# Kernel optimization log

Measured on AMD Instinct MI355X. Metric: run time of the kernel, lower is better.

Reference implementation:

```python
import jax, jax.numpy as jnp
import numpy as np

N = 100000   # nodes (batched graph)
E = 1600000  # edges
G = 2048     # molecules in the batch
D_IN = 128
D_H = 128
MLP_H = 512


def setup_inputs() -> dict:
    key = jax.random.key(0)
    ks = jax.random.split(key, 20)

    def w(k, i, o):
        return (jax.random.normal(k, (i, o), jnp.float32) / np.sqrt(i)).astype(jnp.float32)

    feats = jax.random.normal(ks[0], (N, D_IN), jnp.float32)
    src = jax.random.randint(ks[1], (E,), 0, N)
    dst = jax.random.randint(ks[2], (E,), 0, N)
    graph_ids = jnp.sort(jax.random.randint(ks[3], (N,), 0, G))

    return {
        "feats": feats, "src": src, "dst": dst, "graph_ids": graph_ids,
        # 3 GraphConv layers
        "W0": w(ks[4], D_IN, D_H), "b0": jnp.zeros((D_H,), jnp.float32),
        "W1": w(ks[5], D_H, D_H),  "b1": jnp.zeros((D_H,), jnp.float32),
        "W2": w(ks[6], D_H, D_H),  "b2": jnp.zeros((D_H,), jnp.float32),
        # MLP head: D_H -> 512 -> 256 -> 1
        "Wm0": w(ks[7], D_H, MLP_H),       "bm0": jnp.zeros((MLP_H,), jnp.float32),
        "Wm1": w(ks[8], MLP_H, MLP_H // 2), "bm1": jnp.zeros((MLP_H // 2,), jnp.float32),
        "Wm2": w(ks[9], MLP_H // 2, 1),     "bm2": jnp.zeros((1,), jnp.float32),
    }


def reference(feats, src, dst, graph_ids, W0, b0, W1, b1, W2, b2,
              Wm0, bm0, Wm1, bm1, Wm2, bm2):
    ones_e = jnp.ones((E,), jnp.float32)
    # DGL GraphConv norm='both': D_out^{-1/2} on src, D_in^{-1/2} on dst; deg clamped to 1
    deg_out = jnp.maximum(jax.ops.segment_sum(ones_e, src, num_segments=N), 1.0)
    deg_in = jnp.maximum(jax.ops.segment_sum(ones_e, dst, num_segments=N), 1.0)
    inv_src = jax.lax.rsqrt(deg_out)[:, None]
    inv_dst = jax.lax.rsqrt(deg_in)[:, None]

    def gcn_layer(h, W, b):
        h = h * inv_src                                   # [N, D]
        m = jax.ops.segment_sum(h[src], dst, num_segments=N)  # gather-scatter over edges
        m = m * inv_dst
        return jax.nn.relu(jnp.dot(m, W) + b)

    h = gcn_layer(feats, W0, b0)
    h = gcn_layer(h, W1, b1)
    h = gcn_layer(h, W2, b2)

    # AvgPooling per graph
    counts = jnp.maximum(jax.ops.segment_sum(jnp.ones((N,), jnp.float32), graph_ids, num_segments=G), 1.0)
    emb = jax.ops.segment_sum(h, graph_ids, num_segments=G) / counts[:, None]  # [G, D_H]

    # MLP head (dropout = identity in eval)
    x = jax.nn.relu(jnp.dot(emb, Wm0) + bm0)
    x = jax.nn.relu(jnp.dot(x, Wm1) + bm1)
    return jnp.dot(x, Wm2) + bm2  # [G, 1]
```

## Files before the change

kernel.cpp:

```cpp
#include <hip/hip_runtime.h>


static inline int ceil_div(int a, int b){ return (a + b - 1) / b; }

#define B1 256
#define NBMAX 1024
#define CHUNK_MAX 7168
#define BUCKET_MAX 4096
#define WPREP_BLOCKS 192

typedef __bf16 bf16x8 __attribute__((ext_vector_type(8)));
typedef float  f32x4  __attribute__((ext_vector_type(4)));

static __device__ inline __bf16 bits_to_bf16(unsigned short u){
  union { unsigned short u; __bf16 b; } x; x.u = u; return x.b;
}
static __device__ inline unsigned short bf16_bits(__bf16 b){
  union { __bf16 b; unsigned short u; } x; x.b = b; return x.u;
}
static __device__ inline unsigned pack_split(float s){
  __bf16 h = (__bf16)s;
  __bf16 l = (__bf16)(s - (float)h);
  return ((unsigned)bf16_bits(h) << 16) | (unsigned)bf16_bits(l);
}

__global__ __launch_bounds__(256) void scatter_count_kernel(
    const int* __restrict__ src, const int* __restrict__ dst,
    unsigned* __restrict__ cntA, unsigned* __restrict__ cntB,
    unsigned* __restrict__ stagedA, unsigned char* __restrict__ stagedB,
    const float* __restrict__ W0, const float* __restrict__ W1,
    const float* __restrict__ W2, __bf16* __restrict__ Wsp,
    int E, int NB){
  if (blockIdx.x >= B1){
    int gidx = (blockIdx.x - B1)*256 + threadIdx.x;
    if (gidx < 3*128*128){
      int layer = gidx >> 14, idx = gidx & 16383;
      const float* W = layer == 0 ? W0 : (layer == 1 ? W1 : W2);
      int k = idx >> 7, n = idx & 127;
      float w = W[idx];
      __bf16 h = (__bf16)w;
      __bf16 l = (__bf16)(w - (float)h);
      Wsp[(size_t)layer*2*16384 + n*128 + k] = h;
      Wsp[(size_t)layer*2*16384 + 16384 + n*128 + k] = l;
    }
    return;
  }

  __shared__ unsigned la[NBMAX], lb[NBMAX];
  __shared__ unsigned tsum[256];
  __shared__ unsigned stA[CHUNK_MAX];
  __shared__ unsigned char stB[CHUNK_MAX];

  const int t = threadIdx.x;
  const int blk = blockIdx.x;
  const int chunk = (E + B1 - 1) / B1;
  const int e0 = blk * chunk, e1 = min(e0 + chunk, E);
  const int len = e1 - e0;
  const int strideB = (chunk + 3) & ~3;

  #pragma unroll
  for (int i = t; i < NBMAX; i += 256){ la[i] = 0u; lb[i] = 0u; }
  __syncthreads();
  for (int e = e0 + t; e < e1; e += 256){
    atomicAdd(&la[dst[e] >> 7], 1u);
    atomicAdd(&lb[src[e] >> 7], 1u);
  }
  __syncthreads();

  for (int job = 0; job < 2; job++){
    unsigned* lx = job ? lb : la;
    unsigned* cx = job ? cntB : cntA;
    int b4 = t*4;
    unsigned v0 = lx[b4], v1 = lx[b4+1], v2 = lx[b4+2], v3 = lx[b4+3];
    unsigned s = v0+v1+v2+v3;
    tsum[t] = s;
    __syncthreads();
    for (int off = 1; off < 256; off <<= 1){
      unsigned u = (t >= off) ? tsum[t-off] : 0u;
      __syncthreads();
      tsum[t] += u;
      __syncthreads();
    }
    unsigned run = tsum[t] - s;
    unsigned o0 = run, o1 = run+v0, o2 = run+v0+v1, o3 = run+v0+v1+v2;
    lx[b4] = o0; lx[b4+1] = o1; lx[b4+2] = o2; lx[b4+3] = o3;
    if (b4   < NB) cx[(size_t)blk*NB + b4  ] = o0;
    if (b4+1 < NB) cx[(size_t)blk*NB + b4+1] = o1;
    if (b4+2 < NB) cx[(size_t)blk*NB + b4+2] = o2;
    if (b4+3 < NB) cx[(size_t)blk*NB + b4+3] = o3;
    __syncthreads();
  }

  for (int e = e0 + t; e < e1; e += 256){
    int s = src[e], d = dst[e];
    unsigned pA = atomicAdd(&la[d >> 7], 1u);
    stA[pA] = ((unsigned)(d & 127) << 17) | (unsigned)s;
    unsigned pB = atomicAdd(&lb[s >> 7], 1u);
    stB[pB] = (unsigned char)(s & 127);
  }
  __syncthreads();

  for (int i = t; i < len; i += 256)
    stagedA[(size_t)blk*chunk + i] = stA[i];
  int w4 = (len + 3) >> 2;
  unsigned* gB = (unsigned*)(stagedB + (size_t)blk*strideB);
  for (int i = t; i < w4; i += 256)
    gB[i] = *(unsigned*)&stB[4*i];
}

__global__ void totals_kernel(const unsigned* __restrict__ cntA,
                              const unsigned* __restrict__ cntB,
                              unsigned* __restrict__ totals, int NB, int E){
  int b = blockIdx.x * 256 + threadIdx.x;
  if (b >= NB) return;
  const unsigned* cx = blockIdx.y ? cntB : cntA;
  const int chunk = (E + B1 - 1) / B1;
  unsigned run = 0;
  for (int blk = 0; blk < B1; blk++){
    int lenb = E - blk*chunk; if (lenb > chunk) lenb = chunk; if (lenb < 0) lenb = 0;
    unsigned cur = cx[(size_t)blk*NB + b];
    unsigned nxt = (b < NB-1) ? cx[(size_t)blk*NB + b + 1] : (unsigned)lenb;
    run += nxt - cur;
  }
  totals[(size_t)blockIdx.y*NB + b] = run;
}

__global__ void scan_base_kernel(const unsigned* __restrict__ totals,
                                 unsigned* __restrict__ baseA, unsigned* __restrict__ baseB,
                                 int NB, int E){
  __shared__ unsigned s[NBMAX];
  int t = threadIdx.x;
  for (int job = 0; job < 2; job++){
    unsigned* base = job ? baseB : baseA;
    unsigned x = (t < NB) ? totals[(size_t)job*NB + t] : 0u;
    s[t] = x;
    __syncthreads();
    for (int off = 1; off < NBMAX; off <<= 1){
      unsigned v = (t >= off) ? s[t - off] : 0u;
      __syncthreads();
      s[t] += v;
      __syncthreads();
    }
    if (t < NB) base[t] = s[t] - x;
    if (t == 0) base[NB] = (unsigned)E;
    __syncthreads();
  }
}

__global__ __launch_bounds__(256) void csr_finalize_kernel(
    const unsigned* __restrict__ stagedA, const unsigned char* __restrict__ stagedB,
    const unsigned* __restrict__ cntA, const unsigned* __restrict__ cntB,
    const unsigned* __restrict__ baseA,
    int* __restrict__ row_ptr, float* __restrict__ inv_dst, float* __restrict__ inv_src,
    int* __restrict__ col, int N, int E, int NB){
  __shared__ unsigned offs[256];
  __shared__ unsigned segbase[257];
  __shared__ unsigned tsum[256];
  __shared__ unsigned edge[BUCKET_MAX];
  __shared__ unsigned sorted[BUCKET_MAX];
  __shared__ unsigned cnt[128];
  __shared__ unsigned scn[128];

  const int b = blockIdx.x, t = threadIdx.x;
  const int node0 = b << 7;
  const int nn = min(128, N - node0);
  const int chunk = (E + B1 - 1) / B1;
  const int strideB = (chunk + 3) & ~3;
  int lenb_t = E - t*chunk; if (lenb_t > chunk) lenb_t = chunk; if (lenb_t < 0) lenb_t = 0;

  {
    unsigned o0 = cntA[(size_t)t*NB + b];
    unsigned o1 = (b < NB-1) ? cntA[(size_t)t*NB + b + 1] : (unsigned)lenb_t;
    unsigned len = o1 - o0;
    offs[t] = o0;
    tsum[t] = len;
    __syncthreads();
    for (int off = 1; off < 256; off <<= 1){
      unsigned u = (t >= off) ? tsum[t-off] : 0u;
      __syncthreads();
      tsum[t] += u;
      __syncthreads();
    }
    segbase[t] = tsum[t] - len;
    if (t == 255) segbase[256] = tsum[255];
    __syncthreads();
    int bucketlen = (int)segbase[256];

    for (int idx = t; idx < bucketlen; idx += 256){
      int lo = 0, hi = 255;
      while (lo < hi){ int m = (lo + hi + 1) >> 1; if (segbase[m] <= (unsigned)idx) lo = m; else hi = m - 1; }
      edge[idx] = stagedA[(size_t)lo*chunk + offs[lo] + ((unsigned)idx - segbase[lo])];
    }
    if (t < 128) cnt[t] = 0u;
    __syncthreads();
    for (int idx = t; idx < bucketlen; idx += 256)
      atomicAdd(&cnt[(edge[idx] >> 17) & 127u], 1u);
    __syncthreads();
    unsigned mycnt = (t < 128) ? cnt[t] : 0u;
    if (t < 128) scn[t] = mycnt;
    __syncthreads();
    for (int off = 1; off < 128; off <<= 1){
      unsigned v = (t < 128 && t >= off) ? scn[t - off] : 0u;
      __syncthreads();
      if (t < 128) scn[t] += v;
      __syncthreads();
    }
    int e0 = (int)baseA[b];
    if (t < nn){
      unsigned excl = scn[t] - mycnt;
      row_ptr[node0 + t] = e0 + (int)excl;
      unsigned c = mycnt < 1u ? 1u : mycnt;
      inv_dst[node0 + t] = rsqrtf((float)c);
      cnt[t] = excl;
    }
    if (b == NB - 1 && t == 0) row_ptr[N] = E;
    __syncthreads();
    for (int idx = t; idx < bucketlen; idx += 256){
      unsigned v = edge[idx];
      unsigned p = atomicAdd(&cnt[(v >> 17) & 127u], 1u);
      sorted[p] = v & 0x1FFFFu;
    }
    __syncthreads();
    for (int idx = t; idx < bucketlen; idx += 256)
      col[e0 + idx] = (int)sorted[idx];
  }

  __syncthreads();
  {
    unsigned o0 = cntB[(size_t)t*NB + b];
    unsigned o1 = (b < NB-1) ? cntB[(size_t)t*NB + b + 1] : (unsigned)lenb_t;
    unsigned len = o1 - o0;
    offs[t] = o0;
    tsum[t] = len;
    __syncthreads();
    for (int off = 1; off < 256; off <<= 1){
      unsigned u = (t >= off) ? tsum[t-off] : 0u;
      __syncthreads();
      tsum[t] += u;
      __syncthreads();
    }
    segbase[t] = tsum[t] - len;
    if (t == 255) segbase[256] = tsum[255];
    if (t < 128) cnt[t] = 0u;
    __syncthreads();
    int bucketlen = (int)segbase[256];
    unsigned char* edgeB = (unsigned char*)edge;
    for (int idx = t; idx < bucketlen; idx += 256){
      int lo = 0, hi = 255;
      while (lo < hi){ int m = (lo + hi + 1) >> 1; if (segbase[m] <= (unsigned)idx) lo = m; else hi = m - 1; }
      edgeB[idx] = stagedB[(size_t)lo*strideB + offs[lo] + ((unsigned)idx - segbase[lo])];
    }
    __syncthreads();
    for (int idx = t; idx < bucketlen; idx += 256)
      atomicAdd(&cnt[edgeB[idx]], 1u);
    __syncthreads();
    if (t < nn){
      unsigned c = cnt[t] < 1u ? 1u : cnt[t];
      inv_src[node0 + t] = rsqrtf((float)c);
    }
  }
}

template<bool SC>
__global__ __launch_bounds__(512) void fused_agg_gemm_kernel(
    const int* __restrict__ row_ptr, const int* __restrict__ col,
    const float* __restrict__ hs_in, const float* __restrict__ scale,
    const float* __restrict__ inv_dst,
    const __bf16* __restrict__ Whi, const __bf16* __restrict__ Wlo,
    const float* __restrict__ bias, const float* __restrict__ out_scale,
    float* __restrict__ out, int N){
  __shared__ unsigned Apk[64*132];

  const int tid  = threadIdx.x;
  const int hw   = tid >> 5;
  const int l32  = tid & 31;
  const int row0 = blockIdx.x * 64;

  for (int i = 0; i < 4; i++){
    int j = hw*4 + i;
    int node = row0 + j;
    float4 a0 = make_float4(0.f,0.f,0.f,0.f);
    float4 a1 = make_float4(0.f,0.f,0.f,0.f);
    float4 a2 = make_float4(0.f,0.f,0.f,0.f);
    float4 a3 = make_float4(0.f,0.f,0.f,0.f);
    int e = 0, r1 = 0;
    if (node < N){ e = row_ptr[node]; r1 = row_ptr[node+1]; }
    for (; e + 3 < r1; e += 4){
      int s0 = col[e], s1 = col[e+1], s2 = col[e+2], s3 = col[e+3];
      float4 v0 = ((const float4*)(hs_in + (size_t)s0*128))[l32];
      float4 v1 = ((const float4*)(hs_in + (size_t)s1*128))[l32];
      float4 v2 = ((const float4*)(hs_in + (size_t)s2*128))[l32];
      float4 v3 = ((const float4*)(hs_in + (size_t)s3*128))[l32];
      if (SC){
        float c0 = scale[s0], c1 = scale[s1], c2 = scale[s2], c3 = scale[s3];
        v0.x*=c0; v0.y*=c0; v0.z*=c0; v0.w*=c0;
        v1.x*=c1; v1.y*=c1; v1.z*=c1; v1.w*=c1;
        v2.x*=c2; v2.y*=c2; v2.z*=c2; v2.w*=c2;
        v3.x*=c3; v3.y*=c3; v3.z*=c3; v3.w*=c3;
      }
      a0.x += v0.x; a0.y += v0.y; a0.z += v0.z; a0.w += v0.w;
      a1.x += v1.x; a1.y += v1.y; a1.z += v1.z; a1.w += v1.w;
      a2.x += v2.x; a2.y += v2.y; a2.z += v2.z; a2.w += v2.w;
      a3.x += v3.x; a3.y += v3.y; a3.z += v3.z; a3.w += v3.w;
    }
    for (; e < r1; e++){
      int s0 = col[e];
      float4 v0 = ((const float4*)(hs_in + (size_t)s0*128))[l32];
      if (SC){ float c0 = scale[s0]; v0.x*=c0; v0.y*=c0; v0.z*=c0; v0.w*=c0; }
      a0.x += v0.x; a0.y += v0.y; a0.z += v0.z; a0.w += v0.w;
    }
    float idst = (node < N) ? inv_dst[node] : 0.f;
    float rx = ((a0.x + a1.x) + (a2.x + a3.x)) * idst;
    float ry = ((a0.y + a1.y) + (a2.y + a3.y)) * idst;
    float rz = ((a0.z + a1.z) + (a2.z + a3.z)) * idst;
    float rw = ((a0.w + a1.w) + (a2.w + a3.w)) * idst;
    uint4 p;
    p.x = pack_split(rx); p.y = pack_split(ry);
    p.z = pack_split(rz); p.w = pack_split(rw);
    *(uint4*)&Apk[j*132 + l32*4] = p;
  }
  __syncthreads();

  const int wv   = tid >> 6;
  const int lane = tid & 63;
  const int q    = lane >> 4;
  const int mn   = lane & 15;
  const int mg   = wv >> 2;
  const int ng   = wv & 3;

  f32x4 acc[2][2];
  #pragma unroll
  for (int mt = 0; mt < 2; mt++)
    #pragma unroll
    for (int nt = 0; nt < 2; nt++)
      acc[mt][nt] = (f32x4){0.f,0.f,0.f,0.f};

  #pragma unroll
  for (int kc = 0; kc < 4; kc++){
    bf16x8 ah[2], al[2];
    #pragma unroll
    for (int mt = 0; mt < 2; mt++){
      const unsigned* ap = &Apk[(mg*32 + mt*16 + mn)*132 + kc*32 + q*8];
      uint4 x0 = *(const uint4*)ap;
      uint4 x1 = *(const uint4*)(ap + 4);
      unsigned v[8] = {x0.x, x0.y, x0.z, x0.w, x1.x, x1.y, x1.z, x1.w};
      #pragma unroll
      for (int jj = 0; jj < 8; jj++){
        ah[mt][jj] = bits_to_bf16((unsigned short)(v[jj] >> 16));
        al[mt][jj] = bits_to_bf16((unsigned short)(v[jj] & 0xFFFFu));
      }
    }
    #pragma unroll
    for (int nt = 0; nt < 2; nt++){
      int n = ng*32 + nt*16 + mn;
      const __bf16* bhp = Whi + (size_t)n*128 + kc*32 + q*8;
      const __bf16* blp = Wlo + (size_t)n*128 + kc*32 + q*8;
      bf16x8 bh = *(const bf16x8*)bhp;
      bf16x8 bl = *(const bf16x8*)blp;
      #pragma unroll
      for (int mt = 0; mt < 2; mt++){
        acc[mt][nt] = __builtin_amdgcn_mfma_f32_16x16x32_bf16(al[mt], bh, acc[mt][nt], 0, 0, 0);
        acc[mt][nt] = __builtin_amdgcn_mfma_f32_16x16x32_bf16(ah[mt], bl, acc[mt][nt], 0, 0, 0);
        acc[mt][nt] = __builtin_amdgcn_mfma_f32_16x16x32_bf16(ah[mt], bh, acc[mt][nt], 0, 0, 0);
      }
    }
  }

  #pragma unroll
  for (int mt = 0; mt < 2; mt++){
    #pragma unroll
    for (int r = 0; r < 4; r++){
      int gm = row0 + mg*32 + mt*16 + q*4 + r;
      if (gm < N){
        float osc = out_scale ? out_scale[gm] : 1.f;
        #pragma unroll
        for (int nt = 0; nt < 2; nt++){
          int n = ng*32 + nt*16 + mn;
          float v = acc[mt][nt][r] + bias[n];
          v = fmaxf(v, 0.f) * osc;
          out[(size_t)gm*128 + n] = v;
        }
      }
    }
  }
}

__global__ __launch_bounds__(256) void head_kernel(
    const float* __restrict__ h, const int* __restrict__ gid,
    const float* __restrict__ Wm0, const float* __restrict__ bm0,
    const float* __restrict__ Wm1, const float* __restrict__ bm1,
    const float* __restrict__ Wm2, const float* __restrict__ bm2,
    float* __restrict__ out, int N, int G){
  __shared__ float embL[8][128];
  __shared__ float x1L[8][512];
  __shared__ float x2L[8][256];

  const int t = threadIdx.x;
  const int wave = t >> 6, lane = t & 63;
  const int g0 = blockIdx.x * 8;

  for (int gg = 0; gg < 2; gg++){
    int gl = wave*2 + gg;
    int g = g0 + gl;
    float ax = 0.f, ay = 0.f;
    int start = 0, end = 0;
    if (g < G){
      int lo = 0, hi = N;
      while (lo < hi){ int mid = (lo + hi) >> 1; if (gid[mid] < g) lo = mid + 1; else hi = mid; }
      start = lo;
      hi = N;
      while (lo < hi){ int mid = (lo + hi) >> 1; if (gid[mid] <= g) lo = mid + 1; else hi = mid; }
      end = lo;
      for (int n = start; n < end; n++){
        float2 v = ((const float2*)(h + (size_t)n*128))[lane];
        ax += v.x; ay += v.y;
      }
    }
    int c = end - start; if (c < 1) c = 1;
    float invc = 1.0f / (float)c;
    embL[gl][2*lane]   = ax * invc;
    embL[gl][2*lane+1] = ay * invc;
  }
  __syncthreads();

  {
    float acc[8][2];
    #pragma unroll
    for (int g = 0; g < 8; g++){ acc[g][0] = 0.f; acc[g][1] = 0.f; }
    for (int k = 0; k < 128; k++){
      float w0 = Wm0[(size_t)k*512 + t];
      float w1 = Wm0[(size_t)k*512 + t + 256];
      #pragma unroll
      for (int g = 0; g < 8; g++){
        float e = embL[g][k];
        acc[g][0] = fmaf(e, w0, acc[g][0]);
        acc[g][1] = fmaf(e, w1, acc[g][1]);
      }
    }
    float b0v = bm0[t], b1v = bm0[t + 256];
    #pragma unroll
    for (int g = 0; g < 8; g++){
      x1L[g][t]       = fmaxf(acc[g][0] + b0v, 0.f);
      x1L[g][t + 256] = fmaxf(acc[g][1] + b1v, 0.f);
    }
  }
  __syncthreads();

  {
    float acc[8];
    #pragma unroll
    for (int g = 0; g < 8; g++) acc[g] = 0.f;
    for (int k = 0; k < 512; k++){
      float w = Wm1[(size_t)k*256 + t];
      #pragma unroll
      for (int g = 0; g < 8; g++)
        acc[g] = fmaf(x1L[g][k], w, acc[g]);
    }
    float bv = bm1[t];
    #pragma unroll
    for (int g = 0; g < 8; g++)
      x2L[g][t] = fmaxf(acc[g] + bv, 0.f);
  }
  __syncthreads();

  {
    int g = t >> 5;
    int c = t & 31;
    float s = 0.f;
    for (int i = c; i < 256; i += 32)
      s = fmaf(x2L[g][i], Wm2[i], s);
    for (int off = 16; off > 0; off >>= 1) s += __shfl_down(s, off, 32);
    if (c == 0 && (g0 + g) < G) out[g0 + g] = s + bm2[0];
  }
}

extern "C" void kernel_launch(void* const* d_in, const int* in_sizes, int n_in,
                              void* d_out, int out_size, void* d_ws, size_t ws_size,
                              hipStream_t stream){
  const float* feats = (const float*)d_in[0];
  const int*   src   = (const int*)d_in[1];
  const int*   dst   = (const int*)d_in[2];
  const int*   gid   = (const int*)d_in[3];
  const float* W0 = (const float*)d_in[4];   const float* b0 = (const float*)d_in[5];
  const float* W1 = (const float*)d_in[6];   const float* b1 = (const float*)d_in[7];
  const float* W2 = (const float*)d_in[8];   const float* b2 = (const float*)d_in[9];
  const float* Wm0 = (const float*)d_in[10]; const float* bm0 = (const float*)d_in[11];
  const float* Wm1 = (const float*)d_in[12]; const float* bm1 = (const float*)d_in[13];
  const float* Wm2 = (const float*)d_in[14]; const float* bm2 = (const float*)d_in[15];
  float* out = (float*)d_out;

  const int E   = in_sizes[1];
  const int N   = in_sizes[3];
  const int G   = out_size;
  const int NB  = ceil_div(N, 128);
  const int chunk = ceil_div(E, B1);
  const int strideB = (chunk + 3) & ~3;

  char* ws = (char*)d_ws;
  size_t off = 0;
  auto carve = [&](size_t bytes) -> char* {
    off = (off + 255) & ~(size_t)255;
    char* p = ws + off; off += bytes; return p;
  };
  float* inv_src = (float*)carve((size_t)N*4);
  float* inv_dst = (float*)carve((size_t)N*4);
  int* row_ptr = (int*)carve((size_t)(N+1)*4);
  int* col     = (int*)carve((size_t)E*4);
  __bf16* Wsp = (__bf16*)carve(6*128*128*2);
  float* hsA = (float*)carve((size_t)N*128*4);
  float* hsB = (float*)carve((size_t)N*128*4);

  unsigned* T = (unsigned*)hsB;
  unsigned* cntA   = T;
  unsigned* cntB   = cntA + (size_t)B1*NB;
  unsigned* totals = cntB + (size_t)B1*NB;
  unsigned* baseA  = totals + 2*(size_t)NB;
  unsigned* baseB  = baseA + (NB+1);
  unsigned* stagedA = baseB + (NB+1);
  unsigned char* stagedB = (unsigned char*)(stagedA + (size_t)B1*chunk);

  scatter_count_kernel<<<B1 + WPREP_BLOCKS, 256, 0, stream>>>(
      src, dst, cntA, cntB, stagedA, stagedB, W0, W1, W2, Wsp, E, NB);
  totals_kernel<<<dim3(ceil_div(NB,256), 2), 256, 0, stream>>>(cntA, cntB, totals, NB, E);
  scan_base_kernel<<<1, NBMAX, 0, stream>>>(totals, baseA, baseB, NB, E);
  csr_finalize_kernel<<<NB, 256, 0, stream>>>(stagedA, stagedB, cntA, cntB, baseA,
                                              row_ptr, inv_dst, inv_src, col, N, E, NB);

  const int fgrid = ceil_div(N, 64);
  __bf16 *Whi0 = Wsp,            *Wlo0 = Wsp + 16384;
  __bf16 *Whi1 = Wsp + 2*16384,  *Wlo1 = Wsp + 3*16384;
  __bf16 *Whi2 = Wsp + 4*16384,  *Wlo2 = Wsp + 5*16384;
  fused_agg_gemm_kernel<true><<<fgrid, 512, 0, stream>>>(
      row_ptr, col, feats, inv_src, inv_dst, Whi0, Wlo0, b0, inv_src, hsA, N);
  fused_agg_gemm_kernel<false><<<fgrid, 512, 0, stream>>>(
      row_ptr, col, hsA, nullptr, inv_dst, Whi1, Wlo1, b1, inv_src, hsB, N);
  fused_agg_gemm_kernel<false><<<fgrid, 512, 0, stream>>>(
      row_ptr, col, hsB, nullptr, inv_dst, Whi2, Wlo2, b2, nullptr, hsA, N);
  head_kernel<<<ceil_div(G,8), 256, 0, stream>>>(hsA, gid, Wm0, bm0, Wm1, bm1, Wm2, bm2, out, N, G);
}
```

Before: 701.4 us.

## Use persistent blocks with atomic tile counter and dynamic per-row work queue

The fused aggregation+GEMM kernel now launches a capped persistent grid whose blocks take 64-row tiles from a global atomic counter, reset in the scan kernel. Inside each tile, half-waves take node rows from a shared-memory atomic queue instead of a fixed four rows each. Both changes target load imbalance from varying node degrees. The cost is extra atomics and barriers per tile, and fewer blocks in flight may reduce latency hiding for the random gathers.

```diff
diff --git a/kernel.cpp b/kernel.cpp
--- a/kernel.cpp
+++ b/kernel.cpp
@@ -8,6 +8,7 @@
 #define CHUNK_MAX 7168
 #define BUCKET_MAX 4096
 #define WPREP_BLOCKS 192
+#define PGRID 1024
 
 typedef __bf16 bf16x8 __attribute__((ext_vector_type(8)));
 typedef float  f32x4  __attribute__((ext_vector_type(4)));
@@ -127,9 +128,15 @@
 
 __global__ void scan_base_kernel(const unsigned* __restrict__ totals,
                                  unsigned* __restrict__ baseA, unsigned* __restrict__ baseB,
-                                 int NB, int E){
+                                 unsigned* __restrict__ tile_ctr,
+                                 int NB, int E, int N){
   __shared__ unsigned s[NBMAX];
   int t = threadIdx.x;
+  if (t == 0){
+    unsigned NT = (unsigned)((N + 63) >> 6);
+    unsigned P  = NT < PGRID ? NT : PGRID;
+    tile_ctr[0] = P; tile_ctr[1] = P; tile_ctr[2] = P;
+  }
   for (int job = 0; job < 2; job++){
     unsigned* base = job ? baseB : baseA;
     unsigned x = (t < NB) ? totals[(size_t)job*NB + t] : 0u;
@@ -268,59 +275,13 @@
     const float* __restrict__ inv_dst,
     const __bf16* __restrict__ Whi, const __bf16* __restrict__ Wlo,
     const float* __restrict__ bias, const float* __restrict__ out_scale,
-    float* __restrict__ out, int N){
+    float* __restrict__ out, unsigned* __restrict__ tile_ctr, int N, int NT){
   __shared__ unsigned Apk[64*132];
+  __shared__ int qh;
+  __shared__ int tile_s;
 
   const int tid  = threadIdx.x;
-  const int hw   = tid >> 5;
   const int l32  = tid & 31;
-  const int row0 = blockIdx.x * 64;
-
-  for (int i = 0; i < 4; i++){
-    int j = hw*4 + i;
-    int node = row0 + j;
-    float4 a0 = make_float4(0.f,0.f,0.f,0.f);
-    float4 a1 = make_float4(0.f,0.f,0.f,0.f);
-    float4 a2 = make_float4(0.f,0.f,0.f,0.f);
-    float4 a3 = make_float4(0.f,0.f,0.f,0.f);
-    int e = 0, r1 = 0;
-    if (node < N){ e = row_ptr[node]; r1 = row_ptr[node+1]; }
-    for (; e + 3 < r1; e += 4){
-      int s0 = col[e], s1 = col[e+1], s2 = col[e+2], s3 = col[e+3];
-      float4 v0 = ((const float4*)(hs_in + (size_t)s0*128))[l32];
-      float4 v1 = ((const float4*)(hs_in + (size_t)s1*128))[l32];
-      float4 v2 = ((const float4*)(hs_in + (size_t)s2*128))[l32];
-      float4 v3 = ((const float4*)(hs_in + (size_t)s3*128))[l32];
-      if (SC){
-        float c0 = scale[s0], c1 = scale[s1], c2 = scale[s2], c3 = scale[s3];
-        v0.x*=c0; v0.y*=c0; v0.z*=c0; v0.w*=c0;
-        v1.x*=c1; v1.y*=c1; v1.z*=c1; v1.w*=c1;
-        v2.x*=c2; v2.y*=c2; v2.z*=c2; v2.w*=c2;
-        v3.x*=c3; v3.y*=c3; v3.z*=c3; v3.w*=c3;
-      }
-      a0.x += v0.x; a0.y += v0.y; a0.z += v0.z; a0.w += v0.w;
-      a1.x += v1.x; a1.y += v1.y; a1.z += v1.z; a1.w += v1.w;
-      a2.x += v2.x; a2.y += v2.y; a2.z += v2.z; a2.w += v2.w;
-      a3.x += v3.x; a3.y += v3.y; a3.z += v3.z; a3.w += v3.w;
-    }
-    for (; e < r1; e++){
-      int s0 = col[e];
-      float4 v0 = ((const float4*)(hs_in + (size_t)s0*128))[l32];
-      if (SC){ float c0 = scale[s0]; v0.x*=c0; v0.y*=c0; v0.z*=c0; v0.w*=c0; }
-      a0.x += v0.x; a0.y += v0.y; a0.z += v0.z; a0.w += v0.w;
-    }
-    float idst = (node < N) ? inv_dst[node] : 0.f;
-    float rx = ((a0.x + a1.x) + (a2.x + a3.x)) * idst;
-    float ry = ((a0.y + a1.y) + (a2.y + a3.y)) * idst;
-    float rz = ((a0.z + a1.z) + (a2.z + a3.z)) * idst;
-    float rw = ((a0.w + a1.w) + (a2.w + a3.w)) * idst;
-    uint4 p;
-    p.x = pack_split(rx); p.y = pack_split(ry);
-    p.z = pack_split(rz); p.w = pack_split(rw);
-    *(uint4*)&Apk[j*132 + l32*4] = p;
-  }
-  __syncthreads();
-
   const int wv   = tid >> 6;
   const int lane = tid & 63;
   const int q    = lane >> 4;
@@ -328,60 +289,120 @@
   const int mg   = wv >> 2;
   const int ng   = wv & 3;
 
-  f32x4 acc[2][2];
-  #pragma unroll
-  for (int mt = 0; mt < 2; mt++)
-    #pragma unroll
-    for (int nt = 0; nt < 2; nt++)
-      acc[mt][nt] = (f32x4){0.f,0.f,0.f,0.f};
-
-  #pragma unroll
-  for (int kc = 0; kc < 4; kc++){
-    bf16x8 ah[2], al[2];
-    #pragma unroll
-    for (int mt = 0; mt < 2; mt++){
-      const unsigned* ap = &Apk[(mg*32 + mt*16 + mn)*132 + kc*32 + q*8];
-      uint4 x0 = *(const uint4*)ap;
-      uint4 x1 = *(const uint4*)(ap + 4);
-      unsigned v[8] = {x0.x, x0.y, x0.z, x0.w, x1.x, x1.y, x1.z, x1.w};
+  int tile = blockIdx.x;
+  while (tile < NT){
+    const int row0 = tile * 64;
+
+    if (tid == 0) qh = 0;
+    __syncthreads();
+
+    for (;;){
+      int j = 0;
+      if ((tid & 31) == 0) j = atomicAdd(&qh, 1);
+      j = __shfl(j, 0, 32);
+      if (j >= 64) break;
+      int node = row0 + j;
+      float4 a0 = make_float4(0.f,0.f,0.f,0.f);
+      float4 a1 = make_float4(0.f,0.f,0.f,0.f);
+      float4 a2 = make_float4(0.f,0.f,0.f,0.f);
+      float4 a3 = make_float4(0.f,0.f,0.f,0.f);
+      int e = 0, r1 = 0;
+      if (node < N){ e = row_ptr[node]; r1 = row_ptr[node+1]; }
+      for (; e + 3 < r1; e += 4){
+        int s0 = col[e], s1 = col[e+1], s2 = col[e+2], s3 = col[e+3];
+        float4 v0 = ((const float4*)(hs_in + (size_t)s0*128))[l32];
+        float4 v1 = ((const float4*)(hs_in + (size_t)s1*128))[l32];
+        float4 v2 = ((const float4*)(hs_in + (size_t)s2*128))[l32];
+        float4 v3 = ((const float4*)(hs_in + (size_t)s3*128))[l32];
+        if (SC){
+          float c0 = scale[s0], c1 = scale[s1], c2 = scale[s2], c3 = scale[s3];
+          v0.x*=c0; v0.y*=c0; v0.z*=c0; v0.w*=c0;
+          v1.x*=c1; v1.y*=c1; v1.z*=c1; v1.w*=c1;
+          v2.x*=c2; v2.y*=c2; v2.z*=c2; v2.w*=c2;
+          v3.x*=c3; v3.y*=c3; v3.z*=c3; v3.w*=c3;
+        }
+        a0.x += v0.x; a0.y += v0.y; a0.z += v0.z; a0.w += v0.w;
+        a1.x += v1.x; a1.y += v1.y; a1.z += v1.z; a1.w += v1.w;
+        a2.x += v2.x; a2.y += v2.y; a2.z += v2.z; a2.w += v2.w;
+        a3.x += v3.x; a3.y += v3.y; a3.z += v3.z; a3.w += v3.w;
+      }
+      for (; e < r1; e++){
+        int s0 = col[e];
+        float4 v0 = ((const float4*)(hs_in + (size_t)s0*128))[l32];
+        if (SC){ float c0 = scale[s0]; v0.x*=c0; v0.y*=c0; v0.z*=c0; v0.w*=c0; }
+        a0.x += v0.x; a0.y += v0.y; a0.z += v0.z; a0.w += v0.w;
+      }
+      float idst = (node < N) ? inv_dst[node] : 0.f;
+      float rx = ((a0.x + a1.x) + (a2.x + a3.x)) * idst;
+      float ry = ((a0.y + a1.y) + (a2.y + a3.y)) * idst;
+      float rz = ((a0.z + a1.z) + (a2.z + a3.z)) * idst;
+      float rw = ((a0.w + a1.w) + (a2.w + a3.w)) * idst;
+      uint4 p;
+      p.x = pack_split(rx); p.y = pack_split(ry);
+      p.z = pack_split(rz); p.w = pack_split(rw);
+      *(uint4*)&Apk[j*132 + l32*4] = p;
+    }
+    __syncthreads();
+
+    f32x4 acc[2][2];
+    #pragma unroll
+    for (int mt = 0; mt < 2; mt++)
       #pragma unroll
-      for (int jj = 0; jj < 8; jj++){
-        ah[mt][jj] = bits_to_bf16((unsigned short)(v[jj] >> 16));
-        al[mt][jj] = bits_to_bf16((unsigned short)(v[jj] & 0xFFFFu));
-      }
-    }
-    #pragma unroll
-    for (int nt = 0; nt < 2; nt++){
-      int n = ng*32 + nt*16 + mn;
-      const __bf16* bhp = Whi + (size_t)n*128 + kc*32 + q*8;
-      const __bf16* blp = Wlo + (size_t)n*128 + kc*32 + q*8;
-      bf16x8 bh = *(const bf16x8*)bhp;
-      bf16x8 bl = *(const bf16x8*)blp;
+      for (int nt = 0; nt < 2; nt++)
+        acc[mt][nt] = (f32x4){0.f,0.f,0.f,0.f};
+
+    #pragma unroll
+    for (int kc = 0; kc < 4; kc++){
+      bf16x8 ah[2], al[2];
       #pragma unroll
       for (int mt = 0; mt < 2; mt++){
-        acc[mt][nt] = __builtin_amdgcn_mfma_f32_16x16x32_bf16(al[mt], bh, acc[mt][nt], 0, 0, 0);
-        acc[mt][nt] = __builtin_amdgcn_mfma_f32_16x16x32_bf16(ah[mt], bl, acc[mt][nt], 0, 0, 0);
-        acc[mt][nt] = __builtin_amdgcn_mfma_f32_16x16x32_bf16(ah[mt], bh, acc[mt][nt], 0, 0, 0);
-      }
-    }
-  }
-
-  #pragma unroll
-  for (int mt = 0; mt < 2; mt++){
-    #pragma unroll
-    for (int r = 0; r < 4; r++){
-      int gm = row0 + mg*32 + mt*16 + q*4 + r;
-      if (gm < N){
-        float osc = out_scale ? out_scale[gm] : 1.f;
+        const unsigned* ap = &Apk[(mg*32 + mt*16 + mn)*132 + kc*32 + q*8];
+        uint4 x0 = *(const uint4*)ap;
+        uint4 x1 = *(const uint4*)(ap + 4);
+        unsigned v[8] = {x0.x, x0.y, x0.z, x0.w, x1.x, x1.y, x1.z, x1.w};
         #pragma unroll
-        for (int nt = 0; nt < 2; nt++){
-          int n = ng*32 + nt*16 + mn;
-          float v = acc[mt][nt][r] + bias[n];
-          v = fmaxf(v, 0.f) * osc;
-          out[(size_t)gm*128 + n] = v;
+        for (int jj = 0; jj < 8; jj++){
+          ah[mt][jj] = bits_to_bf16((unsigned short)(v[jj] >> 16));
+          al[mt][jj] = bits_to_bf16((unsigned short)(v[jj] & 0xFFFFu));
         }
       }
-    }
+      #pragma unroll
+      for (int nt = 0; nt < 2; nt++){
+        int n = ng*32 + nt*16 + mn;
+        const __bf16* bhp = Whi + (size_t)n*128 + kc*32 + q*8;
+        const __bf16* blp = Wlo + (size_t)n*128 + kc*32 + q*8;
+        bf16x8 bh = *(const bf16x8*)bhp;
+        bf16x8 bl = *(const bf16x8*)blp;
+        #pragma unroll
+        for (int mt = 0; mt < 2; mt++){
+          acc[mt][nt] = __builtin_amdgcn_mfma_f32_16x16x32_bf16(al[mt], bh, acc[mt][nt], 0, 0, 0);
+          acc[mt][nt] = __builtin_amdgcn_mfma_f32_16x16x32_bf16(ah[mt], bl, acc[mt][nt], 0, 0, 0);
+          acc[mt][nt] = __builtin_amdgcn_mfma_f32_16x16x32_bf16(ah[mt], bh, acc[mt][nt], 0, 0, 0);
+        }
+      }
+    }
+
+    #pragma unroll
+    for (int mt = 0; mt < 2; mt++){
+      #pragma unroll
+      for (int r = 0; r < 4; r++){
+        int gm = row0 + mg*32 + mt*16 + q*4 + r;
+        if (gm < N){
+          float osc = out_scale ? out_scale[gm] : 1.f;
+          #pragma unroll
+          for (int nt = 0; nt < 2; nt++){
+            int n = ng*32 + nt*16 + mn;
+            float v = acc[mt][nt][r] + bias[n];
+            v = fmaxf(v, 0.f) * osc;
+            out[(size_t)gm*128 + n] = v;
+          }
+        }
+      }
+    }
+
+    if (tid == 0) tile_s = (int)atomicAdd(tile_ctr, 1u);
+    __syncthreads();
+    tile = tile_s;
   }
 }
 
@@ -507,6 +528,7 @@
   int* row_ptr = (int*)carve((size_t)(N+1)*4);
   int* col     = (int*)carve((size_t)E*4);
   __bf16* Wsp = (__bf16*)carve(6*128*128*2);
+  unsigned* tctr = (unsigned*)carve(256);
   float* hsA = (float*)carve((size_t)N*128*4);
   float* hsB = (float*)carve((size_t)N*128*4);
 
@@ -522,19 +544,20 @@
   scatter_count_kernel<<<B1 + WPREP_BLOCKS, 256, 0, stream>>>(
       src, dst, cntA, cntB, stagedA, stagedB, W0, W1, W2, Wsp, E, NB);
   totals_kernel<<<dim3(ceil_div(NB,256), 2), 256, 0, stream>>>(cntA, cntB, totals, NB, E);
-  scan_base_kernel<<<1, NBMAX, 0, stream>>>(totals, baseA, baseB, NB, E);
+  scan_base_kernel<<<1, NBMAX, 0, stream>>>(totals, baseA, baseB, tctr, NB, E, N);
   csr_finalize_kernel<<<NB, 256, 0, stream>>>(stagedA, stagedB, cntA, cntB, baseA,
                                               row_ptr, inv_dst, inv_src, col, N, E, NB);
 
-  const int fgrid = ceil_div(N, 64);
+  const int NT = ceil_div(N, 64);
+  const int P  = NT < PGRID ? NT : PGRID;
   __bf16 *Whi0 = Wsp,            *Wlo0 = Wsp + 16384;
   __bf16 *Whi1 = Wsp + 2*16384,  *Wlo1 = Wsp + 3*16384;
   __bf16 *Whi2 = Wsp + 4*16384,  *Wlo2 = Wsp + 5*16384;
-  fused_agg_gemm_kernel<true><<<fgrid, 512, 0, stream>>>(
-      row_ptr, col, feats, inv_src, inv_dst, Whi0, Wlo0, b0, inv_src, hsA, N);
-  fused_agg_gemm_kernel<false><<<fgrid, 512, 0, stream>>>(
-      row_ptr, col, hsA, nullptr, inv_dst, Whi1, Wlo1, b1, inv_src, hsB, N);
-  fused_agg_gemm_kernel<false><<<fgrid, 512, 0, stream>>>(
-      row_ptr, col, hsB, nullptr, inv_dst, Whi2, Wlo2, b2, nullptr, hsA, N);
+  fused_agg_gemm_kernel<true><<<P, 512, 0, stream>>>(
+      row_ptr, col, feats, inv_src, inv_dst, Whi0, Wlo0, b0, inv_src, hsA, tctr+0, N, NT);
+  fused_agg_gemm_kernel<false><<<P, 512, 0, stream>>>(
+      row_ptr, col, hsA, nullptr, inv_dst, Whi1, Wlo1, b1, inv_src, hsB, tctr+1, N, NT);
+  fused_agg_gemm_kernel<false><<<P, 512, 0, stream>>>(
+      row_ptr, col, hsB, nullptr, inv_dst, Whi2, Wlo2, b2, nullptr, hsA, tctr+2, N, NT);
   head_kernel<<<ceil_div(G,8), 256, 0, stream>>>(hsA, gid, Wm0, bm0, Wm1, bm1, Wm2, bm2, out, N, G);
 }
```

New measurement: 776.6 us. +10.7%, slower.
